# Performance work log

Measured on AMD Instinct MI355X. Metric: run time of the kernel, lower is better.

The kernel has to match this reference:

```python
import jax, jax.numpy as jnp
import numpy as np

NUM_EMB = 200_000
DIM = 64
COMPRESSION = 0.25
UPDATE_COUNT = 2
HASHED_SIZE = int(NUM_EMB * DIM * COMPRESSION)  # 3,200,000
NUM_BAGS = 16384
BAG_LEN = 50
TOTAL = NUM_BAGS * BAG_LEN  # 819,200


def setup_inputs() -> dict:
    key = jax.random.key(0)
    k1, k2, k3 = jax.random.split(key, 3)
    # flat indices into the (virtual) [NUM_EMB, DIM] embedding table
    x = jax.random.randint(k1, (TOTAL,), 0, NUM_EMB, dtype=jnp.int32)
    # bag start offsets (equal-size bags of BAG_LEN)
    offsets = jnp.arange(NUM_BAGS, dtype=jnp.int32) * BAG_LEN
    # compressed parameter vector, init U(-sqrt(1/N), sqrt(1/N)) as in the module
    bound = float(np.sqrt(1.0 / NUM_EMB))
    hashed_weight = jax.random.uniform(k2, (HASHED_SIZE,), jnp.float32, -bound, bound)
    # hash index matrices: UPDATE_COUNT tables of shape [NUM_EMB, DIM],
    # values uniform in [0, HASHED_SIZE) (stands in for xxh32(i_j_idxU) % hN)
    weight_idx = jax.random.randint(k3, (UPDATE_COUNT, NUM_EMB, DIM), 0, HASHED_SIZE, dtype=jnp.int32)
    return {"x": x, "offsets": offsets, "hashed_weight": hashed_weight, "weight_idx": weight_idx}


def reference(x, offsets, hashed_weight, weight_idx):
    # Instead of materializing the full dense [NUM_EMB, DIM] table per update
    # (what F.embedding_bag(x, hashed_weight[idx]) does), gather only the rows
    # that x touches: same math, less traffic.
    per_idx = weight_idx[:, x, :]            # [U, T, D] int
    vals = hashed_weight[per_idx]            # [U, T, D]
    tok = vals.sum(axis=0)                   # sum over update_count -> [T, D]
    # embedding_bag 'sum' pooling via segment_sum over bags defined by offsets
    num_bags = offsets.shape[0]
    pos = jnp.arange(x.shape[0], dtype=offsets.dtype)
    seg = jnp.searchsorted(offsets, pos, side='right') - 1  # [T] bag id
    return jax.ops.segment_sum(tok, seg, num_segments=num_bags)  # [B, D]
```

## Files before the change

kernel.cpp:

```cpp
#include <hip/hip_runtime.h>

#define DIM 64
#define K_PASSES 8

typedef int   vint4   __attribute__((ext_vector_type(4)));
typedef float vfloat4 __attribute__((ext_vector_type(4)));

__global__ void emb_sum_kernel(const int* __restrict__ widx,
                               const float* __restrict__ hw,
                               float* __restrict__ esum,
                               long long total ,
                               int hashed_size) {
    long long base = ((long long)blockIdx.x * blockDim.x + threadIdx.x) * 8;
    if (base >= total) return;
    if (base + 8 <= total) {
        const vint4* w0 = (const vint4*)(widx + base);
        const vint4* w1 = (const vint4*)(widx + base + total);
        vint4 a0 = __builtin_nontemporal_load(w0);
        vint4 a1 = __builtin_nontemporal_load(w0 + 1);
        vint4 b0 = __builtin_nontemporal_load(w1);
        vint4 b1 = __builtin_nontemporal_load(w1 + 1);
        int idx[16] = {a0.x, a0.y, a0.z, a0.w, a1.x, a1.y, a1.z, a1.w,
                       b0.x, b0.y, b0.z, b0.w, b1.x, b1.y, b1.z, b1.w};
        float r[16];
#pragma unroll
        for (int i = 0; i < 16; ++i) r[i] = 0.0f;

        int slice = (hashed_size + K_PASSES - 1) / K_PASSES;
        int lo = 0;
        for (int k = 0; k < K_PASSES; ++k, lo += slice) {
#pragma unroll
            for (int i = 0; i < 16; ++i) {
                if ((unsigned)(idx[i] - lo) < (unsigned)slice)
                    r[i] += hw[idx[i]];
            }
        }
        vfloat4 o0 = {r[0] + r[8],  r[1] + r[9],  r[2] + r[10], r[3] + r[11]};
        vfloat4 o1 = {r[4] + r[12], r[5] + r[13], r[6] + r[14], r[7] + r[15]};
        vfloat4* o = (vfloat4*)(esum + base);
        __builtin_nontemporal_store(o0, o);
        __builtin_nontemporal_store(o1, o + 1);
    } else {
        for (long long g = base; g < total; ++g)
            esum[g] = hw[widx[g]] + hw[widx[g + total]];
    }
}

__global__ void bag_sum_kernel(const int* __restrict__ x,
                               const int* __restrict__ offsets,
                               const float* __restrict__ esum,
                               float* __restrict__ out,
                               int num_bags, int total_tokens) {
    int wave = (int)((blockIdx.x * blockDim.x + threadIdx.x) >> 6);
    int lane = threadIdx.x & 63;
    if (wave >= num_bags) return;
    int group = lane >> 4;
    int l16   = lane & 15;
    int start = offsets[wave];
    int end = (wave + 1 < num_bags) ? offsets[wave + 1] : total_tokens;

    vfloat4 acc = {0.0f, 0.0f, 0.0f, 0.0f};
    for (int base = start; base < end; base += 64) {
        int n = end - base;
        if (n > 64) n = 64;
        int xv = (lane < n) ? x[base + lane] : 0;
        int i = 0;
#pragma unroll 4
        for (; i + 4 <= n; i += 4) {
            int e = __shfl(xv, i + group, 64);
            const vfloat4* row = (const vfloat4*)(esum + (size_t)e * DIM);
            acc += row[l16];
        }
        if (i < n) {
            int src = i + group; if (src > n - 1) src = n - 1;
            int e = __shfl(xv, src, 64);
            vfloat4 v = ((const vfloat4*)(esum + (size_t)e * DIM))[l16];
            if (group < n - i) acc += v;
        }
    }
    acc.x += __shfl_xor(acc.x, 16, 64);
    acc.y += __shfl_xor(acc.y, 16, 64);
    acc.z += __shfl_xor(acc.z, 16, 64);
    acc.w += __shfl_xor(acc.w, 16, 64);
    acc.x += __shfl_xor(acc.x, 32, 64);
    acc.y += __shfl_xor(acc.y, 32, 64);
    acc.z += __shfl_xor(acc.z, 32, 64);
    acc.w += __shfl_xor(acc.w, 32, 64);
    if (lane < 16)
        ((vfloat4*)(out + (size_t)wave * DIM))[l16] = acc;
}

__global__ void direct_kernel(const int* __restrict__ x,
                              const int* __restrict__ offsets,
                              const float* __restrict__ hw,
                              const int* __restrict__ widx,
                              float* __restrict__ out,
                              int num_bags, int total_tokens,
                              long long emb_total) {
    int wave = (int)((blockIdx.x * blockDim.x + threadIdx.x) >> 6);
    int lane = threadIdx.x & 63;
    if (wave >= num_bags) return;
    int start = offsets[wave];
    int end = (wave + 1 < num_bags) ? offsets[wave + 1] : total_tokens;

    float acc = 0.0f;
    for (int t = start; t < end; ++t) {
        int e = x[t];
        const int* row = widx + (size_t)e * DIM;
        acc += hw[row[lane]] + hw[row[emb_total + lane]];
    }
    out[(size_t)wave * DIM + lane] = acc;
}

extern "C" void kernel_launch(void* const* d_in, const int* in_sizes, int n_in,
                              void* d_out, int out_size, void* d_ws, size_t ws_size,
                              hipStream_t stream) {
    const int*   x       = (const int*)d_in[0];
    const int*   offsets = (const int*)d_in[1];
    const float* hw      = (const float*)d_in[2];
    const int*   widx    = (const int*)d_in[3];
    float*       out     = (float*)d_out;

    int total_tokens = in_sizes[0];
    int num_bags     = in_sizes[1];
    int hashed_size  = in_sizes[2];
    long long widx_elems = in_sizes[3];
    long long emb_total  = widx_elems / 2;

    size_t need = (size_t)emb_total * sizeof(float);

    if (ws_size >= need) {
        float* esum = (float*)d_ws;
        {
            long long nthreads = (emb_total + 7) / 8;
            int block = 256;
            long long grid = (nthreads + block - 1) / block;
            emb_sum_kernel<<<(int)grid, block, 0, stream>>>(widx, hw, esum,
                                                            emb_total, hashed_size);
        }
        {
            int block = 256;
            int waves_per_block = block / 64;
            int grid = (num_bags + waves_per_block - 1) / waves_per_block;
            bag_sum_kernel<<<grid, block, 0, stream>>>(x, offsets, esum, out,
                                                       num_bags, total_tokens);
        }
    } else {
        int block = 256;
        int waves_per_block = block / 64;
        int grid = (num_bags + waves_per_block - 1) / waves_per_block;
        direct_kernel<<<grid, block, 0, stream>>>(x, offsets, hw, widx, out,
                                                  num_bags, total_tokens, emb_total);
    }
}
```

Before: 346.9 us.

## Store intermediate embedding sums as fp16 and widen per-thread work

The intermediate dense embedding-sum table is now written in half precision instead of fp32. This halves the write traffic in the first kernel and the gather traffic in the bag-sum kernel, which now reads 16-byte chunks of 8 halves and covers eight tokens per wave step. Each thread in the first kernel also handles 16 elements instead of 8, which raises register pressure. Rounding the sums to fp16 adds error to the output.

```diff
diff --git a/kernel.cpp b/kernel.cpp
--- a/kernel.cpp
+++ b/kernel.cpp
@@ -1,93 +1,137 @@
 #include <hip/hip_runtime.h>
+#include <hip/hip_fp16.h>
 
 #define DIM 64
 #define K_PASSES 8
+#define EPT 16
 
-typedef int   vint4   __attribute__((ext_vector_type(4)));
-typedef float vfloat4 __attribute__((ext_vector_type(4)));
+typedef int          vint4   __attribute__((ext_vector_type(4)));
+typedef float        vfloat4 __attribute__((ext_vector_type(4)));
+typedef unsigned int vuint4  __attribute__((ext_vector_type(4)));
+
+static __device__ __forceinline__ float2 h2f2(unsigned u) {
+    __half2 h = __builtin_bit_cast(__half2, u);
+    return __half22float2(h);
+}
 
 __global__ void emb_sum_kernel(const int* __restrict__ widx,
                                const float* __restrict__ hw,
-                               float* __restrict__ esum,
+                               __half* __restrict__ esum,
                                long long total ,
                                int hashed_size) {
-    long long base = ((long long)blockIdx.x * blockDim.x + threadIdx.x) * 8;
+    long long base = ((long long)blockIdx.x * blockDim.x + threadIdx.x) * EPT;
     if (base >= total) return;
-    if (base + 8 <= total) {
+    if (base + EPT <= total) {
+        int idx[2 * EPT];
         const vint4* w0 = (const vint4*)(widx + base);
         const vint4* w1 = (const vint4*)(widx + base + total);
-        vint4 a0 = __builtin_nontemporal_load(w0);
-        vint4 a1 = __builtin_nontemporal_load(w0 + 1);
-        vint4 b0 = __builtin_nontemporal_load(w1);
-        vint4 b1 = __builtin_nontemporal_load(w1 + 1);
-        int idx[16] = {a0.x, a0.y, a0.z, a0.w, a1.x, a1.y, a1.z, a1.w,
-                       b0.x, b0.y, b0.z, b0.w, b1.x, b1.y, b1.z, b1.w};
-        float r[16];
 #pragma unroll
-        for (int i = 0; i < 16; ++i) r[i] = 0.0f;
+        for (int q = 0; q < EPT / 4; ++q) {
+            vint4 a = __builtin_nontemporal_load(w0 + q);
+            idx[4 * q + 0] = a.x; idx[4 * q + 1] = a.y;
+            idx[4 * q + 2] = a.z; idx[4 * q + 3] = a.w;
+        }
+#pragma unroll
+        for (int q = 0; q < EPT / 4; ++q) {
+            vint4 b = __builtin_nontemporal_load(w1 + q);
+            idx[EPT + 4 * q + 0] = b.x; idx[EPT + 4 * q + 1] = b.y;
+            idx[EPT + 4 * q + 2] = b.z; idx[EPT + 4 * q + 3] = b.w;
+        }
+        float r[2 * EPT];
+#pragma unroll
+        for (int i = 0; i < 2 * EPT; ++i) r[i] = 0.0f;
 
         int slice = (hashed_size + K_PASSES - 1) / K_PASSES;
         int lo = 0;
         for (int k = 0; k < K_PASSES; ++k, lo += slice) {
 #pragma unroll
-            for (int i = 0; i < 16; ++i) {
+            for (int i = 0; i < 2 * EPT; ++i) {
                 if ((unsigned)(idx[i] - lo) < (unsigned)slice)
                     r[i] += hw[idx[i]];
             }
         }
-        vfloat4 o0 = {r[0] + r[8],  r[1] + r[9],  r[2] + r[10], r[3] + r[11]};
-        vfloat4 o1 = {r[4] + r[12], r[5] + r[13], r[6] + r[14], r[7] + r[15]};
-        vfloat4* o = (vfloat4*)(esum + base);
-        __builtin_nontemporal_store(o0, o);
-        __builtin_nontemporal_store(o1, o + 1);
+        unsigned u[EPT / 2];
+#pragma unroll
+        for (int p = 0; p < EPT / 2; ++p) {
+            float s0 = r[2 * p] + r[EPT + 2 * p];
+            float s1 = r[2 * p + 1] + r[EPT + 2 * p + 1];
+            __half2 h = __halves2half2(__float2half_rn(s0), __float2half_rn(s1));
+            u[p] = __builtin_bit_cast(unsigned, h);
+        }
+        vuint4* o = (vuint4*)(esum + base);
+        vuint4 o0 = {u[0], u[1], u[2], u[3]};
+        vuint4 o1 = {u[4], u[5], u[6], u[7]};
+        o[0] = o0;
+        o[1] = o1;
     } else {
         for (long long g = base; g < total; ++g)
-            esum[g] = hw[widx[g]] + hw[widx[g + total]];
+            esum[g] = __float2half_rn(hw[widx[g]] + hw[widx[g + total]]);
     }
 }
 
 __global__ void bag_sum_kernel(const int* __restrict__ x,
                                const int* __restrict__ offsets,
-                               const float* __restrict__ esum,
+                               const __half* __restrict__ esum,
                                float* __restrict__ out,
                                int num_bags, int total_tokens) {
     int wave = (int)((blockIdx.x * blockDim.x + threadIdx.x) >> 6);
     int lane = threadIdx.x & 63;
     if (wave >= num_bags) return;
-    int group = lane >> 4;
-    int l16   = lane & 15;
+    int group = lane >> 3;
+    int l8    = lane & 7;
     int start = offsets[wave];
     int end = (wave + 1 < num_bags) ? offsets[wave + 1] : total_tokens;
 
-    vfloat4 acc = {0.0f, 0.0f, 0.0f, 0.0f};
+    float2 acc0 = {0.f, 0.f}, acc1 = {0.f, 0.f}, acc2 = {0.f, 0.f}, acc3 = {0.f, 0.f};
     for (int base = start; base < end; base += 64) {
         int n = end - base;
         if (n > 64) n = 64;
         int xv = (lane < n) ? x[base + lane] : 0;
         int i = 0;
-#pragma unroll 4
-        for (; i + 4 <= n; i += 4) {
+#pragma unroll 2
+        for (; i + 8 <= n; i += 8) {
             int e = __shfl(xv, i + group, 64);
-            const vfloat4* row = (const vfloat4*)(esum + (size_t)e * DIM);
-            acc += row[l16];
+            vuint4 v = ((const vuint4*)(esum + (size_t)e * DIM))[l8];
+            float2 f0 = h2f2(v.x);
+            float2 f1 = h2f2(v.y);
+            float2 f2 = h2f2(v.z);
+            float2 f3 = h2f2(v.w);
+            acc0.x += f0.x; acc0.y += f0.y;
+            acc1.x += f1.x; acc1.y += f1.y;
+            acc2.x += f2.x; acc2.y += f2.y;
+            acc3.x += f3.x; acc3.y += f3.y;
         }
         if (i < n) {
+            int r = n - i;
             int src = i + group; if (src > n - 1) src = n - 1;
             int e = __shfl(xv, src, 64);
-            vfloat4 v = ((const vfloat4*)(esum + (size_t)e * DIM))[l16];
-            if (group < n - i) acc += v;
+            vuint4 v = ((const vuint4*)(esum + (size_t)e * DIM))[l8];
+            if (group < r) {
+                float2 f0 = h2f2(v.x);
+                float2 f1 = h2f2(v.y);
+                float2 f2 = h2f2(v.z);
+                float2 f3 = h2f2(v.w);
+                acc0.x += f0.x; acc0.y += f0.y;
+                acc1.x += f1.x; acc1.y += f1.y;
+                acc2.x += f2.x; acc2.y += f2.y;
+                acc3.x += f3.x; acc3.y += f3.y;
+            }
         }
     }
-    acc.x += __shfl_xor(acc.x, 16, 64);
-    acc.y += __shfl_xor(acc.y, 16, 64);
-    acc.z += __shfl_xor(acc.z, 16, 64);
-    acc.w += __shfl_xor(acc.w, 16, 64);
-    acc.x += __shfl_xor(acc.x, 32, 64);
-    acc.y += __shfl_xor(acc.y, 32, 64);
-    acc.z += __shfl_xor(acc.z, 32, 64);
-    acc.w += __shfl_xor(acc.w, 32, 64);
-    if (lane < 16)
-        ((vfloat4*)(out + (size_t)wave * DIM))[l16] = acc;
+#pragma unroll
+    for (int m = 8; m <= 32; m <<= 1) {
+        acc0.x += __shfl_xor(acc0.x, m, 64); acc0.y += __shfl_xor(acc0.y, m, 64);
+        acc1.x += __shfl_xor(acc1.x, m, 64); acc1.y += __shfl_xor(acc1.y, m, 64);
+        acc2.x += __shfl_xor(acc2.x, m, 64); acc2.y += __shfl_xor(acc2.y, m, 64);
+        acc3.x += __shfl_xor(acc3.x, m, 64); acc3.y += __shfl_xor(acc3.y, m, 64);
+    }
+    if (lane < 8) {
+        vfloat4* orow = (vfloat4*)(out + (size_t)wave * DIM);
+        vfloat4 p0 = {acc0.x, acc0.y, acc1.x, acc1.y};
+        vfloat4 p1 = {acc2.x, acc2.y, acc3.x, acc3.y};
+        orow[l8 * 2]     = p0;
+        orow[l8 * 2 + 1] = p1;
+    }
 }
 
 __global__ void direct_kernel(const int* __restrict__ x,
@@ -127,12 +171,12 @@
     long long widx_elems = in_sizes[3];
     long long emb_total  = widx_elems / 2;
 
-    size_t need = (size_t)emb_total * sizeof(float);
+    size_t need = (size_t)emb_total * sizeof(__half);
 
     if (ws_size >= need) {
-        float* esum = (float*)d_ws;
+        __half* esum = (__half*)d_ws;
         {
-            long long nthreads = (emb_total + 7) / 8;
+            long long nthreads = (emb_total + EPT - 1) / EPT;
             int block = 256;
             long long grid = (nthreads + block - 1) / block;
             emb_sum_kernel<<<(int)grid, block, 0, stream>>>(widx, hw, esum,
```

Result: slower. 455.7 us (+31.3%).
